# Kernel tuning notes

Hardware: AMD Instinct MI355X
Metric: run time of the kernel (lower is better)

Reference implementation:

```python
import jax, jax.numpy as jnp
import numpy as np

N_NODES = 50000


def setup_inputs() -> dict:
    key = jax.random.key(0)
    ks = jax.random.split(key, 6)
    d_in, d_out = 256, 256
    n_edges = 1_600_000
    x = jax.random.normal(ks[0], (N_NODES, d_in), dtype=jnp.float32)
    edge_index = jax.random.randint(ks[1], (2, n_edges), 0, N_NODES, dtype=jnp.int64)
    edge_attr = jax.random.normal(ks[2], (n_edges, 16), dtype=jnp.float32)  # unused by forward
    W1 = jax.random.normal(ks[3], (d_in, d_out), dtype=jnp.float32) * (1.0 / np.sqrt(d_in))
    b1 = jnp.zeros((d_out,), dtype=jnp.float32)
    W2 = jax.random.normal(ks[4], (d_out, d_out), dtype=jnp.float32) * (1.0 / np.sqrt(d_out))
    b2 = jnp.zeros((d_out,), dtype=jnp.float32)
    eps = jnp.zeros((1,), dtype=jnp.float32)  # train_eps=True, init 0
    return {"x": x, "edge_index": edge_index, "edge_attr": edge_attr,
            "W1": W1, "b1": b1, "W2": W2, "b2": b2, "eps": eps}


def reference(x, edge_index, edge_attr, W1, b1, W2, b2, eps):
    src, dst = edge_index[0], edge_index[1]
    # sum aggregation: agg[i] = sum_{(j->i) in E} x[j]
    agg = jax.ops.segment_sum(x[src], dst, num_segments=N_NODES)  # [N, d_in]
    h = (1.0 + eps[0]) * x + agg
    # MLP: Linear -> ReLU -> (dropout=0) -> Linear
    h = jax.nn.relu(h @ W1 + b1)
    out = h @ W2 + b2
    return out
```

## Files before the change

### kernel.cpp

```cpp
#include <hip/hip_runtime.h>
#include <stdint.h>

#define NODES 50000
#define D 256
#define MP 50048
#define NBUCK 196
#define CAP 10240
#define EPB 4096
#define HS_LD 264
#define CAST_BLOCKS 12500

typedef short bf16x8 __attribute__((ext_vector_type(8)));
typedef float f32x4 __attribute__((ext_vector_type(4)));

__device__ inline unsigned short f2b(float f) {
    unsigned int u = __float_as_uint(f);
    unsigned int r = (u + 0x7fffu + ((u >> 16) & 1u)) >> 16;
    return (unsigned short)r;
}

__device__ inline bool ei_is64(const int* ei) {
    return (ei[1] | ei[3] | ei[5] | ei[7]) == 0;
}
__device__ inline int ei_get(const int* __restrict__ ei, long long pos, bool is64) {
    return is64 ? ei[2 * pos] : ei[(int)pos];
}

__global__ __launch_bounds__(256) void prep_kernel(const float* __restrict__ x,
                                                   unsigned short* __restrict__ xb,
                                                   int* __restrict__ bcnt,
                                                   const float* __restrict__ W1,
                                                   const float* __restrict__ W2,
                                                   unsigned short* __restrict__ P1,
                                                   unsigned short* __restrict__ P2,
                                                   int* __restrict__ offs, int E) {
    int blk = blockIdx.x;
    if (blk < CAST_BLOCKS) {
        if (blk == 0 && threadIdx.x < NBUCK) bcnt[threadIdx.x] = 0;
        if (blk == 0 && threadIdx.x == 0) offs[NODES] = E;
        int t = blk * 256 + threadIdx.x;
        float4 v = ((const float4*)x)[t];
        unsigned int lo = (unsigned int)f2b(v.x) | ((unsigned int)f2b(v.y) << 16);
        unsigned int hi = (unsigned int)f2b(v.z) | ((unsigned int)f2b(v.w) << 16);
        ((uint2*)xb)[t] = make_uint2(lo, hi);
    } else {
        int t = (blk - CAST_BLOCKS) * 256 + threadIdx.x;
        const float* W = (t < 8192) ? W1 : W2;
        unsigned short* P = (t < 8192) ? P1 : P2;
        int u = t & 8191;
        int lane = u & 63, nt = (u >> 6) & 15, s = u >> 10;
        int q = lane >> 4, n = nt * 16 + (lane & 15);
        int kbase = s * 32 + q * 8;
#pragma unroll
        for (int j = 0; j < 8; j++) P[u * 8 + j] = f2b(W[(kbase + j) * D + n]);
    }
}

__global__ __launch_bounds__(256) void partA_kernel(const int* __restrict__ ei, int E,
                                                    int* __restrict__ bcnt,
                                                    unsigned int* __restrict__ ebufT) {
    __shared__ int cnt[256];
    __shared__ int incl[256];
    __shared__ int lcur[256];
    __shared__ int gbase[256];
    __shared__ unsigned int stage[EPB];
    bool is64 = ei_is64(ei);
    int tid = threadIdx.x;
    cnt[tid] = 0;
    __syncthreads();
    long long pairBase = ((long long)blockIdx.x * EPB) >> 1;
    unsigned int w[16];
    int bk[16];
#pragma unroll
    for (int r = 0; r < 8; r++) {
        long long pp = pairBase + (long long)r * 256 + tid;
        long long e0 = pp * 2;
        int s0 = 0, s1 = 0, d0 = 0, d1 = 0;
        bool v1 = (e0 + 1 < E), v0 = (e0 < E);
        if (v1) {
            if (is64) {
                uint4 sv = *(const uint4*)(ei + 4 * pp);
                uint4 dv = *(const uint4*)(ei + (size_t)2 * E + 4 * pp);
                s0 = (int)sv.x; s1 = (int)sv.z; d0 = (int)dv.x; d1 = (int)dv.z;
            } else {
                uint2 sv = *(const uint2*)(ei + 2 * pp);
                uint2 dv = *(const uint2*)(ei + (size_t)E + 2 * pp);
                s0 = (int)sv.x; s1 = (int)sv.y; d0 = (int)dv.x; d1 = (int)dv.y;
            }
        } else if (v0) {
            s0 = ei_get(ei, e0, is64);
            d0 = ei_get(ei, (long long)E + e0, is64);
        }
        bk[2 * r] = v0 ? (d0 >> 8) : 255;
        bk[2 * r + 1] = v1 ? (d1 >> 8) : 255;
        w[2 * r] = ((unsigned int)bk[2 * r] << 24) |
                   ((unsigned int)(d0 & 255) << 16) | (unsigned int)s0;
        w[2 * r + 1] = ((unsigned int)bk[2 * r + 1] << 24) |
                       ((unsigned int)(d1 & 255) << 16) | (unsigned int)s1;
        atomicAdd(&cnt[bk[2 * r]], 1);
        atomicAdd(&cnt[bk[2 * r + 1]], 1);
    }
    __syncthreads();
    int c = cnt[tid];
    incl[tid] = c;
    __syncthreads();
    for (int off = 1; off < 256; off <<= 1) {
        int xv = (tid >= off) ? incl[tid - off] : 0;
        __syncthreads();
        incl[tid] += xv;
        __syncthreads();
    }
    if (tid < NBUCK && c > 0) gbase[tid] = atomicAdd(&bcnt[tid], c);
    lcur[tid] = incl[tid] - c;
    __syncthreads();
#pragma unroll
    for (int r = 0; r < 16; r++) {
        int p = atomicAdd(&lcur[bk[r]], 1);
        stage[p] = w[r];
    }
    __syncthreads();
    for (int i = tid; i < EPB; i += 256) {
        unsigned int u = stage[i];
        int b = u >> 24;
        if (b < NBUCK) {
            int slot = gbase[b] + (i - (incl[b] - cnt[b]));
            ebufT[(size_t)b * CAP + slot] = u & 0x00FFFFFFu;
        }
    }
}

__global__ __launch_bounds__(1024) void partB_kernel(const int* __restrict__ bcnt,
                                                     const unsigned int* __restrict__ ebufT,
                                                     int* __restrict__ offs,
                                                     int* __restrict__ ebuf) {
    __shared__ int sb[256];
    __shared__ int ncnt[2048];
    __shared__ int ncur[2048];
    __shared__ int nexcl[256];
    int b = blockIdx.x, tid = threadIdx.x;
    if (tid < 256) sb[tid] = (tid < NBUCK) ? bcnt[tid] : 0;
    for (int i = tid; i < 2048; i += 1024) ncnt[i] = 0;
    __syncthreads();
    for (int off = 1; off < 256; off <<= 1) {
        int xv = 0;
        if (tid < 256 && tid >= off) xv = sb[tid - off];
        __syncthreads();
        if (tid < 256) sb[tid] += xv;
        __syncthreads();
    }
    int n = bcnt[b];
    int base = sb[b] - n;
    const unsigned int* reg = ebufT + (size_t)b * CAP;
    for (int i = tid; i < n; i += 1024) {
        unsigned int w = reg[i];
        atomicAdd(&ncnt[((w >> 16) << 3) | ((w & 0xffffu) >> 13)], 1);
    }
    __syncthreads();
    if (tid < 256) {
        int s = 0;
#pragma unroll
        for (int c = 0; c < 8; c++) s += ncnt[tid * 8 + c];
        nexcl[tid] = s;
    }
    __syncthreads();
    for (int off = 1; off < 256; off <<= 1) {
        int xv = 0;
        if (tid < 256 && tid >= off) xv = nexcl[tid - off];
        __syncthreads();
        if (tid < 256) nexcl[tid] += xv;
        __syncthreads();
    }
    if (tid < 256) {
        int s = 0;
#pragma unroll
        for (int c = 0; c < 8; c++) s += ncnt[tid * 8 + c];
        int excl = nexcl[tid] - s;
        int node = b * 256 + tid;
        if (node < NODES) offs[node] = base + excl;
        int run = excl;
#pragma unroll
        for (int c = 0; c < 8; c++) {
            ncur[tid * 8 + c] = run;
            run += ncnt[tid * 8 + c];
        }
    }
    __syncthreads();
    for (int i = tid; i < n; i += 1024) {
        unsigned int w = reg[i];
        int p = atomicAdd(&ncur[((w >> 16) << 3) | ((w & 0xffffu) >> 13)], 1);
        ebuf[base + p] = (int)(w & 0xffffu);
    }
}

__device__ inline void upk2(uint2 w, float* a) {
    a[0] += __uint_as_float(w.x << 16);
    a[1] += __uint_as_float(w.x & 0xffff0000u);
    a[2] += __uint_as_float(w.y << 16);
    a[3] += __uint_as_float(w.y & 0xffff0000u);
}

__global__ __launch_bounds__(256) void agg_kernel(const unsigned short* __restrict__ xb,
                                                  const int* __restrict__ offs,
                                                  const int* __restrict__ ebuf,
                                                  const float* __restrict__ eps,
                                                  unsigned short* __restrict__ h0) {
    int wv = (blockIdx.x * 256 + threadIdx.x) >> 6;
    if (wv >= NODES) return;
    int lane = threadIdx.x & 63;
    const unsigned short* colBase = xb + lane * 4;
    float aa[4] = {0, 0, 0, 0}, bb[4] = {0, 0, 0, 0};
    int beg = offs[wv], end = offs[wv + 1];
    int j = beg;
    for (; j + 8 <= end; j += 8) {
        int idx[8];
        uint2 g[8];
#pragma unroll
        for (int k = 0; k < 8; k++) idx[k] = ebuf[j + k];
#pragma unroll
        for (int k = 0; k < 8; k++) g[k] = *(const uint2*)(colBase + (size_t)idx[k] * D);
#pragma unroll
        for (int k = 0; k < 8; k += 2) {
            upk2(g[k], aa);
            upk2(g[k + 1], bb);
        }
    }
    if (j + 4 <= end) {
        int idx[4];
        uint2 g[4];
#pragma unroll
        for (int k = 0; k < 4; k++) idx[k] = ebuf[j + k];
#pragma unroll
        for (int k = 0; k < 4; k++) g[k] = *(const uint2*)(colBase + (size_t)idx[k] * D);
#pragma unroll
        for (int k = 0; k < 4; k += 2) {
            upk2(g[k], aa);
            upk2(g[k + 1], bb);
        }
        j += 4;
    }
    for (; j < end; ++j) {
        uint2 g = *(const uint2*)(colBase + (size_t)ebuf[j] * D);
        upk2(g, aa);
    }
    float scale = 1.0f + eps[0];
    uint2 v = *(const uint2*)(colBase + (size_t)wv * D);
    aa[0] += scale * __uint_as_float(v.x << 16);
    aa[1] += scale * __uint_as_float(v.x & 0xffff0000u);
    aa[2] += scale * __uint_as_float(v.y << 16);
    aa[3] += scale * __uint_as_float(v.y & 0xffff0000u);
    unsigned int lo = (unsigned int)f2b(aa[0] + bb[0]) | ((unsigned int)f2b(aa[1] + bb[1]) << 16);
    unsigned int hi = (unsigned int)f2b(aa[2] + bb[2]) | ((unsigned int)f2b(aa[3] + bb[3]) << 16);
    *(uint2*)(h0 + (size_t)wv * D + lane * 4) = make_uint2(lo, hi);
}

__global__ __launch_bounds__(256) void gemm_fused_kernel(const unsigned short* __restrict__ A,
                                                         const unsigned short* __restrict__ P1,
                                                         const float* __restrict__ b1,
                                                         const unsigned short* __restrict__ P2,
                                                         const float* __restrict__ b2,
                                                         float* __restrict__ out, int Mvalid) {
    __shared__ unsigned short hs[64 * HS_LD];
    int wv = threadIdx.x >> 6;
    int lane = threadIdx.x & 63;
    int quad = lane >> 4, l16 = lane & 15;
    int mBase = blockIdx.x * 64;
    const bf16x8* B1v = (const bf16x8*)P1;
    const bf16x8* B2v = (const bf16x8*)P2;

    {
        f32x4 acc[4][4] = {};
#pragma unroll
        for (int ks = 0; ks < 8; ks++) {
            bf16x8 af[4], bf[4];
#pragma unroll
            for (int mi = 0; mi < 4; mi++) {
                int row = mBase + mi * 16 + l16;
                af[mi] = *(const bf16x8*)(A + (size_t)row * D + ks * 32 + quad * 8);
            }
#pragma unroll
            for (int ni = 0; ni < 4; ni++) bf[ni] = B1v[(ks * 16 + wv * 4 + ni) * 64 + lane];
#pragma unroll
            for (int mi = 0; mi < 4; mi++)
#pragma unroll
                for (int ni = 0; ni < 4; ni++)
                    acc[mi][ni] = __builtin_amdgcn_mfma_f32_16x16x32_bf16(af[mi], bf[ni],
                                                                          acc[mi][ni], 0, 0, 0);
        }
#pragma unroll
        for (int mi = 0; mi < 4; mi++)
#pragma unroll
            for (int ni = 0; ni < 4; ni++) {
                int col = wv * 64 + ni * 16 + l16;
                float bs = b1[col];
#pragma unroll
                for (int r = 0; r < 4; r++) {
                    int rl = mi * 16 + quad * 4 + r;
                    hs[rl * HS_LD + col] = f2b(fmaxf(acc[mi][ni][r] + bs, 0.0f));
                }
            }
    }
    __syncthreads();

    f32x4 acc[4][4] = {};
#pragma unroll
    for (int ks = 0; ks < 8; ks++) {
        bf16x8 af[4], bf[4];
#pragma unroll
        for (int mi = 0; mi < 4; mi++)
            af[mi] = *(const bf16x8*)(hs + (mi * 16 + l16) * HS_LD + ks * 32 + quad * 8);
#pragma unroll
        for (int ni = 0; ni < 4; ni++) bf[ni] = B2v[(ks * 16 + wv * 4 + ni) * 64 + lane];
#pragma unroll
        for (int mi = 0; mi < 4; mi++)
#pragma unroll
            for (int ni = 0; ni < 4; ni++)
                acc[mi][ni] =
                    __builtin_amdgcn_mfma_f32_16x16x32_bf16(af[mi], bf[ni], acc[mi][ni], 0, 0, 0);
    }
#pragma unroll
    for (int mi = 0; mi < 4; mi++)
#pragma unroll
        for (int ni = 0; ni < 4; ni++) {
            int col = wv * 64 + ni * 16 + l16;
            float bs = b2[col];
#pragma unroll
            for (int r = 0; r < 4; r++) {
                int row = mBase + mi * 16 + quad * 4 + r;
                if (row < Mvalid) out[(size_t)row * D + col] = acc[mi][ni][r] + bs;
            }
        }
}

extern "C" void kernel_launch(void* const* d_in, const int* in_sizes, int n_in,
                              void* d_out, int out_size, void* d_ws, size_t ws_size,
                              hipStream_t stream) {
    const float* x = (const float*)d_in[0];
    const int* ei = (const int*)d_in[1];
    const float* W1 = (const float*)d_in[3];
    const float* b1 = (const float*)d_in[4];
    const float* W2 = (const float*)d_in[5];
    const float* b2 = (const float*)d_in[6];
    const float* eps = (const float*)d_in[7];
    int E = in_sizes[1] / 2;

    char* p = (char*)d_ws;
    auto alloc = [&](size_t bytes) {
        char* r = p;
        p += (bytes + 255) & ~(size_t)255;
        return r;
    };
    unsigned short* xb = (unsigned short*)alloc((size_t)MP * D * 2);
    unsigned short* h0 = (unsigned short*)alloc((size_t)MP * D * 2);
    unsigned short* P1 = (unsigned short*)alloc(8192 * 8 * 2);
    unsigned short* P2 = (unsigned short*)alloc(8192 * 8 * 2);
    int* bcnt = (int*)alloc((size_t)NBUCK * 4);
    int* offs = (int*)alloc((size_t)(NODES + 1) * 4);
    int* ebuf = (int*)alloc((size_t)E * 4);
    unsigned int* ebufT = (unsigned int*)alloc((size_t)NBUCK * CAP * 4);

    prep_kernel<<<CAST_BLOCKS + 64, 256, 0, stream>>>(x, xb, bcnt, W1, W2, P1, P2, offs, E);
    partA_kernel<<<(E + EPB - 1) / EPB, 256, 0, stream>>>(ei, E, bcnt, ebufT);
    partB_kernel<<<NBUCK, 1024, 0, stream>>>(bcnt, ebufT, offs, ebuf);
    agg_kernel<<<(NODES + 3) / 4, 256, 0, stream>>>(xb, offs, ebuf, eps, h0);
    gemm_fused_kernel<<<MP / 64, 256, 0, stream>>>(h0, P1, b1, P2, b2, (float*)d_out, NODES);
}
```

Measured before the change: 360.2 us.

## Phase aggregation by source-node range so concurrent gathers share a cache-resident slice

```diff
diff --git a/kernel.cpp b/kernel.cpp
--- a/kernel.cpp
+++ b/kernel.cpp
@@ -9,6 +9,8 @@
 #define EPB 4096
 #define HS_LD 264
 #define CAST_BLOCKS 12500
+#define AGG_BLOCKS 2048
+#define NPW 7
 
 typedef short bf16x8 __attribute__((ext_vector_type(8)));
 typedef float f32x4 __attribute__((ext_vector_type(4)));
@@ -33,11 +35,11 @@
                                                    const float* __restrict__ W2,
                                                    unsigned short* __restrict__ P1,
                                                    unsigned short* __restrict__ P2,
-                                                   int* __restrict__ offs, int E) {
+                                                   int* __restrict__ offs2, int E) {
     int blk = blockIdx.x;
     if (blk < CAST_BLOCKS) {
         if (blk == 0 && threadIdx.x < NBUCK) bcnt[threadIdx.x] = 0;
-        if (blk == 0 && threadIdx.x == 0) offs[NODES] = E;
+        if (blk == 0 && threadIdx.x == 0) offs2[NODES * 8] = E;
         int t = blk * 256 + threadIdx.x;
         float4 v = ((const float4*)x)[t];
         unsigned int lo = (unsigned int)f2b(v.x) | ((unsigned int)f2b(v.y) << 16);
@@ -131,7 +133,7 @@
 
 __global__ __launch_bounds__(1024) void partB_kernel(const int* __restrict__ bcnt,
                                                      const unsigned int* __restrict__ ebufT,
-                                                     int* __restrict__ offs,
+                                                     int* __restrict__ offs2,
                                                      int* __restrict__ ebuf) {
     __shared__ int sb[256];
     __shared__ int ncnt[2048];
@@ -176,11 +178,11 @@
         for (int c = 0; c < 8; c++) s += ncnt[tid * 8 + c];
         int excl = nexcl[tid] - s;
         int node = b * 256 + tid;
-        if (node < NODES) offs[node] = base + excl;
         int run = excl;
 #pragma unroll
         for (int c = 0; c < 8; c++) {
             ncur[tid * 8 + c] = run;
+            if (node < NODES) offs2[node * 8 + c] = base + run;
             run += ncnt[tid * 8 + c];
         }
     }
@@ -199,58 +201,67 @@
     a[3] += __uint_as_float(w.y & 0xffff0000u);
 }
 
-__global__ __launch_bounds__(256) void agg_kernel(const unsigned short* __restrict__ xb,
-                                                  const int* __restrict__ offs,
-                                                  const int* __restrict__ ebuf,
-                                                  const float* __restrict__ eps,
-                                                  unsigned short* __restrict__ h0) {
-    int wv = (blockIdx.x * 256 + threadIdx.x) >> 6;
-    if (wv >= NODES) return;
+__global__ __launch_bounds__(256, 8) void agg_kernel(const unsigned short* __restrict__ xb,
+                                                     const int* __restrict__ offs2,
+                                                     const int* __restrict__ ebuf,
+                                                     const float* __restrict__ eps,
+                                                     unsigned short* __restrict__ h0) {
+    int W = (blockIdx.x << 2) | (threadIdx.x >> 6);
     int lane = threadIdx.x & 63;
     const unsigned short* colBase = xb + lane * 4;
-    float aa[4] = {0, 0, 0, 0}, bb[4] = {0, 0, 0, 0};
-    int beg = offs[wv], end = offs[wv + 1];
-    int j = beg;
-    for (; j + 8 <= end; j += 8) {
-        int idx[8];
-        uint2 g[8];
-#pragma unroll
-        for (int k = 0; k < 8; k++) idx[k] = ebuf[j + k];
-#pragma unroll
-        for (int k = 0; k < 8; k++) g[k] = *(const uint2*)(colBase + (size_t)idx[k] * D);
-#pragma unroll
-        for (int k = 0; k < 8; k += 2) {
-            upk2(g[k], aa);
-            upk2(g[k + 1], bb);
-        }
-    }
-    if (j + 4 <= end) {
-        int idx[4];
-        uint2 g[4];
-#pragma unroll
-        for (int k = 0; k < 4; k++) idx[k] = ebuf[j + k];
-#pragma unroll
-        for (int k = 0; k < 4; k++) g[k] = *(const uint2*)(colBase + (size_t)idx[k] * D);
-#pragma unroll
-        for (int k = 0; k < 4; k += 2) {
-            upk2(g[k], aa);
-            upk2(g[k + 1], bb);
-        }
-        j += 4;
-    }
-    for (; j < end; ++j) {
-        uint2 g = *(const uint2*)(colBase + (size_t)ebuf[j] * D);
-        upk2(g, aa);
-    }
+    float acc[NPW][4];
+#pragma unroll
+    for (int t = 0; t < NPW; t++)
+        acc[t][0] = acc[t][1] = acc[t][2] = acc[t][3] = 0.0f;
     float scale = 1.0f + eps[0];
-    uint2 v = *(const uint2*)(colBase + (size_t)wv * D);
-    aa[0] += scale * __uint_as_float(v.x << 16);
-    aa[1] += scale * __uint_as_float(v.x & 0xffff0000u);
-    aa[2] += scale * __uint_as_float(v.y << 16);
-    aa[3] += scale * __uint_as_float(v.y & 0xffff0000u);
-    unsigned int lo = (unsigned int)f2b(aa[0] + bb[0]) | ((unsigned int)f2b(aa[1] + bb[1]) << 16);
-    unsigned int hi = (unsigned int)f2b(aa[2] + bb[2]) | ((unsigned int)f2b(aa[3] + bb[3]) << 16);
-    *(uint2*)(h0 + (size_t)wv * D + lane * 4) = make_uint2(lo, hi);
+
+    for (int c = 0; c < 8; ++c) {
+#pragma unroll
+        for (int t = 0; t < NPW; ++t) {
+            int node = W + (t << 13);
+            if (node < NODES) {
+                int beg = offs2[node * 8 + c];
+                int end = offs2[node * 8 + c + 1];
+                if ((node >> 13) == c) {
+                    uint2 v = *(const uint2*)(colBase + (size_t)node * D);
+                    acc[t][0] += scale * __uint_as_float(v.x << 16);
+                    acc[t][1] += scale * __uint_as_float(v.x & 0xffff0000u);
+                    acc[t][2] += scale * __uint_as_float(v.y << 16);
+                    acc[t][3] += scale * __uint_as_float(v.y & 0xffff0000u);
+                }
+                int j = beg;
+                for (; j + 4 <= end; j += 4) {
+                    int i0 = ebuf[j], i1 = ebuf[j + 1], i2 = ebuf[j + 2], i3 = ebuf[j + 3];
+                    uint2 g0 = *(const uint2*)(colBase + (size_t)i0 * D);
+                    uint2 g1 = *(const uint2*)(colBase + (size_t)i1 * D);
+                    uint2 g2 = *(const uint2*)(colBase + (size_t)i2 * D);
+                    uint2 g3 = *(const uint2*)(colBase + (size_t)i3 * D);
+                    upk2(g0, acc[t]);
+                    upk2(g1, acc[t]);
+                    upk2(g2, acc[t]);
+                    upk2(g3, acc[t]);
+                }
+                for (; j < end; ++j) {
+                    uint2 g = *(const uint2*)(colBase + (size_t)ebuf[j] * D);
+                    upk2(g, acc[t]);
+                }
+            }
+        }
+    }
+#pragma unroll
+    for (int t = 0; t < NPW; ++t) {
+        int node = W + (t << 13);
+        if (node < NODES) {
+            unsigned long long packed =
+                (unsigned long long)((unsigned int)f2b(acc[t][0]) |
+                                     ((unsigned int)f2b(acc[t][1]) << 16)) |
+                ((unsigned long long)((unsigned int)f2b(acc[t][2]) |
+                                      ((unsigned int)f2b(acc[t][3]) << 16))
+                 << 32);
+            __builtin_nontemporal_store(
+                packed, (unsigned long long*)(h0 + (size_t)node * D + lane * 4));
+        }
+    }
 }
 
 __global__ __launch_bounds__(256) void gemm_fused_kernel(const unsigned short* __restrict__ A,
@@ -354,13 +365,13 @@
     unsigned short* P1 = (unsigned short*)alloc(8192 * 8 * 2);
     unsigned short* P2 = (unsigned short*)alloc(8192 * 8 * 2);
     int* bcnt = (int*)alloc((size_t)NBUCK * 4);
-    int* offs = (int*)alloc((size_t)(NODES + 1) * 4);
+    int* offs2 = (int*)alloc((size_t)(NODES * 8 + 1) * 4);
     int* ebuf = (int*)alloc((size_t)E * 4);
     unsigned int* ebufT = (unsigned int*)alloc((size_t)NBUCK * CAP * 4);
 
-    prep_kernel<<<CAST_BLOCKS + 64, 256, 0, stream>>>(x, xb, bcnt, W1, W2, P1, P2, offs, E);
+    prep_kernel<<<CAST_BLOCKS + 64, 256, 0, stream>>>(x, xb, bcnt, W1, W2, P1, P2, offs2, E);
     partA_kernel<<<(E + EPB - 1) / EPB, 256, 0, stream>>>(ei, E, bcnt, ebufT);
-    partB_kernel<<<NBUCK, 1024, 0, stream>>>(bcnt, ebufT, offs, ebuf);
-    agg_kernel<<<(NODES + 3) / 4, 256, 0, stream>>>(xb, offs, ebuf, eps, h0);
+    partB_kernel<<<NBUCK, 1024, 0, stream>>>(bcnt, ebufT, offs2, ebuf);
+    agg_kernel<<<AGG_BLOCKS, 256, 0, stream>>>(xb, offs2, ebuf, eps, h0);
     gemm_fused_kernel<<<MP / 64, 256, 0, stream>>>(h0, P1, b1, P2, b2, (float*)d_out, NODES);
 }
```

Measured after the change: 383.1 us. 1.06x slower.
